# Kernel optimization log

Measured on AMD Instinct MI355X. Metric: run time of the kernel, lower is better.

## Reference

```python
import jax, jax.numpy as jnp
import numpy as np

B, T, V, DIN = 16, 360, 25, 2
H, NCLS, NAUX = 128, 12, 8
NSPLITS = NAUX + 1
N = T * V        # nodes per graph
E = 72000        # edges per graph
EPS = 1e-5       # BatchNorm eps


def _norm_coefs(edge_index, n):
    # GCNConv default: add self-loops, symmetric normalization D^-1/2 (A+I) D^-1/2
    src, dst = edge_index[0], edge_index[1]
    loops = jnp.arange(n, dtype=src.dtype)
    src = jnp.concatenate([src, loops])
    dst = jnp.concatenate([dst, loops])
    deg = jnp.zeros((n,), jnp.float32).at[dst].add(1.0)
    dinv = jax.lax.rsqrt(deg)
    return src, dst, dinv[src] * dinv[dst]


def _gcn_bn_relu(x, W, b, gamma, beta, src, dst, coef):
    # x: [B, N, din] -> [B, N, dout]; GCNConv then BatchNorm1d (batch stats) + ReLU
    h = x @ W
    msg = h[:, src, :] * coef[None, :, None]          # gather + scale
    agg = jnp.zeros(h.shape, h.dtype).at[:, dst, :].add(msg) + b  # scatter-add
    mean = agg.mean(axis=(0, 1))
    var = agg.var(axis=(0, 1))                        # biased var, as torch BN fwd
    hn = (agg - mean) * jax.lax.rsqrt(var + EPS)
    return jax.nn.relu(gamma * hn + beta)


def _head(x, Wg, bg, gamma, beta, Wf, bf, src, dst, coef):
    h = _gcn_bn_relu(x, Wg, bg, gamma, beta, src, dst, coef)
    pooled = h.mean(axis=1)                           # GlobalMeanPool (equal-size graphs)
    # Dropout is identity in eval mode
    return jax.nn.log_softmax(pooled @ Wf + bf, axis=1)


def setup_inputs() -> dict:
    key = jax.random.key(0)
    ks = jax.random.split(key, 8)
    s = 0.1
    return {
        "x": jax.random.normal(ks[0], (B, T, V, DIN), jnp.float32),
        "edge_index": jax.random.randint(ks[1], (2, E), 0, N, jnp.int64 if jax.config.jax_enable_x64 else jnp.int32),
        "W_in": jax.random.normal(ks[2], (DIN, H), jnp.float32) * s,
        "b_in": jnp.zeros((H,), jnp.float32),
        "g_in": jnp.ones((H,), jnp.float32),
        "be_in": jnp.zeros((H,), jnp.float32),
        "shared_W": jax.random.normal(ks[3], (2, H, H), jnp.float32) * s,
        "shared_b": jnp.zeros((2, H), jnp.float32),
        "shared_g": jnp.ones((2, H), jnp.float32),
        "shared_be": jnp.zeros((2, H), jnp.float32),
        "main_Wg": jax.random.normal(ks[4], (H, H), jnp.float32) * s,
        "main_bg": jnp.zeros((H,), jnp.float32),
        "main_g": jnp.ones((H,), jnp.float32),
        "main_be": jnp.zeros((H,), jnp.float32),
        "main_Wf": jax.random.normal(ks[5], (H, NCLS), jnp.float32) * s,
        "main_bf": jnp.zeros((NCLS,), jnp.float32),
        "aux_Wg": jax.random.normal(ks[6], (NAUX, H, H), jnp.float32) * s,
        "aux_bg": jnp.zeros((NAUX, H), jnp.float32),
        "aux_g": jnp.ones((NAUX, H), jnp.float32),
        "aux_be": jnp.zeros((NAUX, H), jnp.float32),
        "aux_Wf": jax.random.normal(ks[7], (NAUX, H, NCLS), jnp.float32) * s,
        "aux_bf": jnp.zeros((NAUX, NCLS), jnp.float32),
    }


def reference(x, edge_index, W_in, b_in, g_in, be_in, shared_W, shared_b, shared_g,
              shared_be, main_Wg, main_bg, main_g, main_be, main_Wf, main_bf,
              aux_Wg, aux_bg, aux_g, aux_be, aux_Wf, aux_bf):
    src, dst, coef = _norm_coefs(edge_index, N)
    h = x.reshape(B, N, DIN)
    h = _gcn_bn_relu(h, W_in, b_in, g_in, be_in, src, dst, coef)
    for i in range(shared_W.shape[0]):
        h = _gcn_bn_relu(h, shared_W[i], shared_b[i], shared_g[i], shared_be[i], src, dst, coef)
    o_main = _head(h, main_Wg, main_bg, main_g, main_be, main_Wf, main_bf, src, dst, coef)
    h4 = h.reshape(B, T, V, H)
    ws = T // NSPLITS
    t = jnp.arange(T)
    outs = []
    for i in range(NSPLITS - 1):
        idx = (t + ws * (i + 1)) % T          # cyclic time shift (fi[si:si+T])
        hr = h4[:, idx].reshape(B, N, H)
        outs.append(_head(hr, aux_Wg[i], aux_bg[i], aux_g[i], aux_be[i],
                          aux_Wf[i], aux_bf[i], src, dst, coef))
    o_aux = jnp.stack(outs, axis=1)           # [B, NAUX, NCLS]
    return o_main, o_aux
```

## Files before the change

### kernel.cpp

```cpp
#include <hip/hip_runtime.h>
#include <hip/hip_bf16.h>
#include <math.h>

#define BB 16
#define TT 360
#define VV 25
#define NN 9000
#define EE 72000
#define HH 128
#define RR (NN * BB)
#define CROWS 18000
#define NT128 1125
#define NPART0 563
#define NCLSS 12
#define EPSB 1e-5f


typedef _Float16 h8v __attribute__((ext_vector_type(8)));
typedef float float16v __attribute__((ext_vector_type(16)));

__device__ __forceinline__ h8v cf8(unsigned packed) {
    uint4 cc = {packed, packed, packed, packed};
    return __builtin_bit_cast(h8v, cc);
}


__global__ void k_count(const int* __restrict__ ei, int* __restrict__ counts) {
    int e = blockIdx.x * 256 + threadIdx.x;
    if (e < EE) atomicAdd(&counts[ei[EE + e]], 1);
}

__global__ void k_dinv(const int* __restrict__ counts, float* __restrict__ dinv,
                       unsigned* __restrict__ d2p) {
    int n = blockIdx.x * 256 + threadIdx.x;
    if (n >= NN) return;
    float di = rsqrtf((float)(counts[n] + 1));
    dinv[n] = di;
    _Float16 d2 = (_Float16)(di * di);
    unsigned short u = __builtin_bit_cast(unsigned short, d2);
    d2p[n] = (unsigned)u | ((unsigned)u << 16);
}

__global__ void k_scan(const int* __restrict__ counts, int* __restrict__ rowptr4) {
    __shared__ int part[1024];
    int t = threadIdx.x;
    int base = t * 9;
    int loc[9];
    int s = 0;
#pragma unroll
    for (int i = 0; i < 9; i++) {
        int idx = base + i;
        int v = (idx < NN) ? ((counts[idx] + 3) & ~3) : 0;
        loc[i] = s;
        s += v;
    }
    part[t] = s;
    __syncthreads();
    for (int d = 1; d < 1024; d <<= 1) {
        int v = (t >= d) ? part[t - d] : 0;
        __syncthreads();
        part[t] += v;
        __syncthreads();
    }
    int excl = (t == 0) ? 0 : part[t - 1];
#pragma unroll
    for (int i = 0; i < 9; i++) {
        int idx = base + i;
        if (idx < NN) rowptr4[idx] = excl + loc[i];
    }
    if (t == 1023) rowptr4[NN] = part[1023];
}

__global__ void k_fill(const int* __restrict__ ei, const int* __restrict__ rowptr4,
                       int* __restrict__ cursor, const float* __restrict__ dinv,
                       int2* __restrict__ csr) {
    int e = blockIdx.x * 256 + threadIdx.x;
    if (e >= EE) return;
    int s = ei[e], d = ei[EE + e];
    int slot = rowptr4[d] + atomicAdd(&cursor[d], 1);
    _Float16 cfh = (_Float16)(dinv[s] * dinv[d]);
    unsigned short u = __builtin_bit_cast(unsigned short, cfh);
    int2 e2;
    e2.x = s;
    e2.y = (int)((unsigned)u | ((unsigned)u << 16));
    csr[slot] = e2;
}

__global__ void k_pad(const int* __restrict__ rowptr4, const int* __restrict__ cursor,
                      int2* __restrict__ csr) {
    int n = blockIdx.x * 256 + threadIdx.x;
    if (n >= NN) return;
    int beg = rowptr4[n] + cursor[n];
    int end = rowptr4[n + 1];
    int2 z;
    z.x = n;
    z.y = 0;
    for (int e = beg; e < end; e++) csr[e] = z;
}

__global__ void k_wcvt(const float* __restrict__ sW, const float* __restrict__ mW,
                       const float* __restrict__ aW, _Float16* __restrict__ Wh) {
    int idx = blockIdx.x * 256 + threadIdx.x;
    if (idx >= 11 * 16384) return;
    int l = idx >> 14, r = idx & 16383;
    int k = r >> 7, c = r & 127;
    const float* src = (l < 2) ? sW + (size_t)l * 16384
                               : ((l == 2) ? mW : aW + (size_t)(l - 3) * 16384);
    Wh[(size_t)l * 16384 + c * 128 + k] = (_Float16)src[k * 128 + c];
}

__global__ void k_prop2(const float* __restrict__ x, float* __restrict__ P0,
                        const int* __restrict__ rowptr4, const int2* __restrict__ csr,
                        const float* __restrict__ dinv) {
    int n = blockIdx.x * 256 + threadIdx.x;
    if (n >= NN) return;
    int b = blockIdx.y;
    const float* xb = x + (size_t)b * NN * 2;
    float d2 = dinv[n] * dinv[n];
    float a0 = d2 * xb[2 * n], a1 = d2 * xb[2 * n + 1];
    int beg = rowptr4[n], end = rowptr4[n + 1];
    for (int j = beg; j < end; j++) {
        int2 e2 = csr[j];
        int s = e2.x;
        unsigned short u = (unsigned short)((unsigned)e2.y & 0xffffu);
        float cf = (float)__builtin_bit_cast(_Float16, u);
        a0 += cf * xb[2 * s];
        a1 += cf * xb[2 * s + 1];
    }
    float* Pb = P0 + (size_t)(n * BB + b) * 2;
    Pb[0] = a0;
    Pb[1] = a1;
}

__global__ void __launch_bounds__(256) k_mm2(const float* __restrict__ P0,
                                             _Float16* __restrict__ A,
                                             const float* __restrict__ W,
                                             const float* __restrict__ bias,
                                             float* __restrict__ pS1, float* __restrict__ pS2) {
    __shared__ float L1[256][8], L2[256][8];
    int t = threadIdx.x;
    int cg = t & 15, c8 = cg * 8;
    float wv0[8], wv1[8], bv[8];
#pragma unroll
    for (int j = 0; j < 8; j++) {
        wv0[j] = W[c8 + j];
        wv1[j] = W[HH + c8 + j];
        bv[j] = bias[c8 + j];
    }
    float s1[8], s2[8];
#pragma unroll
    for (int j = 0; j < 8; j++) { s1[j] = 0.f; s2[j] = 0.f; }
    for (int idx = blockIdx.x * 256 + t; idx < RR * 16; idx += gridDim.x * 256) {
        int Rr = idx >> 4;
        int q = Rr / CROWS;
        int rr = Rr - q * CROWS;
        int n = rr >> 1;
        int b = q * 2 + (rr & 1);
        float p0 = P0[((size_t)n * BB + b) * 2], p1 = P0[((size_t)n * BB + b) * 2 + 1];
        h8v o;
#pragma unroll
        for (int j = 0; j < 8; j++) {
            float v = p0 * wv0[j] + p1 * wv1[j] + bv[j];
            s1[j] += v;
            s2[j] += v * v;
            o[j] = (_Float16)v;
        }
        *(h8v*)(A + (size_t)Rr * HH + c8) = o;
    }
#pragma unroll
    for (int j = 0; j < 8; j++) { L1[t][j] = s1[j]; L2[t][j] = s2[j]; }
    __syncthreads();
    if (t < 16) {
#pragma unroll
        for (int g = 1; g < 16; g++)
#pragma unroll
            for (int j = 0; j < 8; j++) {
                s1[j] = (g == 1 ? L1[t][j] : s1[j]) + L1[t + 16 * g][j];
                s2[j] = (g == 1 ? L2[t][j] : s2[j]) + L2[t + 16 * g][j];
            }
#pragma unroll
        for (int j = 0; j < 8; j++) {
            pS1[(size_t)(t * 8 + j) * NPART0 + blockIdx.x] = s1[j];
            pS2[(size_t)(t * 8 + j) * NPART0 + blockIdx.x] = s2[j];
        }
    }
}

__global__ void __launch_bounds__(256) k_act(const _Float16* __restrict__ A,
                                             _Float16* __restrict__ HP,
                                             const float* __restrict__ scale,
                                             const float* __restrict__ shiftv) {
    int i = blockIdx.x * 256 + threadIdx.x;
    int c8 = (i & 15) * 8;
    h8v v = *(const h8v*)(A + (size_t)i * 8);
    h8v o;
#pragma unroll
    for (int j = 0; j < 8; j++) {
        float f = (float)v[j] * scale[c8 + j] + shiftv[c8 + j];
        o[j] = (_Float16)fmaxf(f, 0.f);
    }
    *(h8v*)(HP + (size_t)i * 8) = o;
}

__global__ void __launch_bounds__(256) k_gather1(const _Float16* __restrict__ h,
                                                 _Float16* __restrict__ Pz,
                                                 const int* __restrict__ rowptr4,
                                                 const int2* __restrict__ csr,
                                                 const unsigned* __restrict__ d2p) {
    int t = threadIdx.x;
    int q = blockIdx.x & 7;
    int ng4 = blockIdx.x >> 3;
    int wv = t >> 6, l = t & 63;
    int n = ng4 * 4 + wv;
    int half = l >> 5, li = l & 31;
    const _Float16* hb = h + (size_t)q * CROWS * HH + (size_t)li * 8;
    h8v acc;
    {
        h8v v = *(const h8v*)(hb + (size_t)n * 2 * HH);
        acc = v * cf8(half ? 0u : d2p[n]);
    }
    int beg = rowptr4[n], end = rowptr4[n + 1];
    int e = beg;
    for (; e + 8 <= end; e += 8) {
        int4 m0 = *(const int4*)(csr + e);
        int4 m1 = *(const int4*)(csr + e + 2);
        int4 m2 = *(const int4*)(csr + e + 4);
        int4 m3 = *(const int4*)(csr + e + 6);
        int s0 = half ? m0.z : m0.x;
        int s1 = half ? m1.z : m1.x;
        int s2 = half ? m2.z : m2.x;
        int s3 = half ? m3.z : m3.x;
        h8v v0 = *(const h8v*)(hb + (size_t)s0 * 2 * HH);
        h8v v1 = *(const h8v*)(hb + (size_t)s1 * 2 * HH);
        h8v v2 = *(const h8v*)(hb + (size_t)s2 * 2 * HH);
        h8v v3 = *(const h8v*)(hb + (size_t)s3 * 2 * HH);
        acc += v0 * cf8((unsigned)(half ? m0.w : m0.y));
        acc += v1 * cf8((unsigned)(half ? m1.w : m1.y));
        acc += v2 * cf8((unsigned)(half ? m2.w : m2.y));
        acc += v3 * cf8((unsigned)(half ? m3.w : m3.y));
    }
    if (e < end) {
        int4 m0 = *(const int4*)(csr + e);
        int4 m1 = *(const int4*)(csr + e + 2);
        int s0 = half ? m0.z : m0.x;
        int s1 = half ? m1.z : m1.x;
        h8v v0 = *(const h8v*)(hb + (size_t)s0 * 2 * HH);
        h8v v1 = *(const h8v*)(hb + (size_t)s1 * 2 * HH);
        acc += v0 * cf8((unsigned)(half ? m0.w : m0.y));
        acc += v1 * cf8((unsigned)(half ? m1.w : m1.y));
    }
    {
        int4 ai = __builtin_bit_cast(int4, acc);
        int4 bi4;
        bi4.x = __shfl_xor(ai.x, 32, 64);
        bi4.y = __shfl_xor(ai.y, 32, 64);
        bi4.z = __shfl_xor(ai.z, 32, 64);
        bi4.w = __shfl_xor(ai.w, 32, 64);
        acc += __builtin_bit_cast(h8v, bi4);
    }
    if (half == 0) {
        *(h8v*)(Pz + ((size_t)q * CROWS + (size_t)n * 2) * HH + (size_t)li * 8) = acc;
    }
}

__global__ void __launch_bounds__(256) k_gather3c(const _Float16* __restrict__ h,
                                                  _Float16* B0, _Float16* B1, _Float16* B2,
                                                  const int* __restrict__ rowptr4,
                                                  const int2* __restrict__ csr,
                                                  const unsigned* __restrict__ d2p,
                                                  int shbase) {
    int t = threadIdx.x;
    int q = blockIdx.x & 7;
    int ng4 = blockIdx.x >> 3;
    int wv = t >> 6, l = t & 63;
    int n = ng4 * 4 + wv;
    int half = l >> 5, li = l & 31;
    const _Float16* hb = h + (size_t)q * CROWS * HH + (size_t)li * 8;
    int sh0 = shbase, sh1 = shbase + 1000, sh2 = shbase + 2000;
    h8v acc0, acc1, acc2;
    {
        unsigned dp = half ? 0u : d2p[n];
        int p0 = n + sh0; if (p0 >= NN) p0 -= NN;
        int p1 = n + sh1; if (p1 >= NN) p1 -= NN;
        int p2 = n + sh2; if (p2 >= NN) p2 -= NN;
        h8v v0 = *(const h8v*)(hb + (size_t)p0 * 2 * HH);
        h8v v1 = *(const h8v*)(hb + (size_t)p1 * 2 * HH);
        h8v v2 = *(const h8v*)(hb + (size_t)p2 * 2 * HH);
        h8v dv = cf8(dp);
        acc0 = v0 * dv;
        acc1 = v1 * dv;
        acc2 = v2 * dv;
    }
    int beg = rowptr4[n], end = rowptr4[n + 1];
    for (int e = beg; e < end; e += 4) {
        int4 m0 = *(const int4*)(csr + e);
        int4 m1 = *(const int4*)(csr + e + 2);
        int sA = half ? m0.z : m0.x;
        int sB = half ? m1.z : m1.x;
        unsigned cA = (unsigned)(half ? m0.w : m0.y);
        unsigned cB = (unsigned)(half ? m1.w : m1.y);
        int a0 = sA + sh0; if (a0 >= NN) a0 -= NN;
        int a1 = sA + sh1; if (a1 >= NN) a1 -= NN;
        int a2 = sA + sh2; if (a2 >= NN) a2 -= NN;
        int b0 = sB + sh0; if (b0 >= NN) b0 -= NN;
        int b1 = sB + sh1; if (b1 >= NN) b1 -= NN;
        int b2 = sB + sh2; if (b2 >= NN) b2 -= NN;
        h8v vA0 = *(const h8v*)(hb + (size_t)a0 * 2 * HH);
        h8v vA1 = *(const h8v*)(hb + (size_t)a1 * 2 * HH);
        h8v vA2 = *(const h8v*)(hb + (size_t)a2 * 2 * HH);
        h8v vB0 = *(const h8v*)(hb + (size_t)b0 * 2 * HH);
        h8v vB1 = *(const h8v*)(hb + (size_t)b1 * 2 * HH);
        h8v vB2 = *(const h8v*)(hb + (size_t)b2 * 2 * HH);
        h8v fA = cf8(cA), fB = cf8(cB);
        acc0 += vA0 * fA;
        acc1 += vA1 * fA;
        acc2 += vA2 * fA;
        acc0 += vB0 * fB;
        acc1 += vB1 * fB;
        acc2 += vB2 * fB;
    }
#pragma unroll
    for (int z = 0; z < 3; z++) {
        h8v* ap = (z == 0) ? &acc0 : ((z == 1) ? &acc1 : &acc2);
        int4 ai = __builtin_bit_cast(int4, *ap);
        int4 bi4;
        bi4.x = __shfl_xor(ai.x, 32, 64);
        bi4.y = __shfl_xor(ai.y, 32, 64);
        bi4.z = __shfl_xor(ai.z, 32, 64);
        bi4.w = __shfl_xor(ai.w, 32, 64);
        *ap += __builtin_bit_cast(h8v, bi4);
    }
    if (half == 0) {
        size_t off = ((size_t)q * CROWS + (size_t)n * 2) * HH + (size_t)li * 8;
        *(h8v*)(B0 + off) = acc0;
        *(h8v*)(B1 + off) = acc1;
        *(h8v*)(B2 + off) = acc2;
    }
}

__global__ void __launch_bounds__(256) k_mfma3(_Float16* B0, _Float16* B1, _Float16* B2,
                                               const _Float16* __restrict__ Wh_g,
                                               const float* bias0, const float* bias1,
                                               const float* bias2,
                                               float* __restrict__ pS1,
                                               float* __restrict__ pS2) {
    __shared__ float rb1[4][128], rb2[4][128];
    int z = blockIdx.y;
    _Float16* B = (z == 0) ? B0 : ((z == 1) ? B1 : B2);
    const _Float16* Wh = Wh_g + (size_t)z * 16384;
    const float* bias = (z == 0) ? bias0 : ((z == 1) ? bias1 : bias2);
    int t = threadIdx.x;
    int w = t >> 6, l = t & 63;
    int rw = w >> 1, cw = w & 1;
    int lr = l & 31, hi = l >> 5;
    size_t rbase = (size_t)blockIdx.x * 128;
    const _Float16* Pr0 = B + (rbase + rw * 32 + lr) * HH + hi * 8;
    const _Float16* Pr1 = B + (rbase + 64 + rw * 32 + lr) * HH + hi * 8;
    const _Float16* Wc0 = Wh + (size_t)(cw * 64 + lr) * HH + hi * 8;
    const _Float16* Wc1 = Wh + (size_t)(cw * 64 + 32 + lr) * HH + hi * 8;
    float16v acc2[2][2];
#pragma unroll
    for (int rt = 0; rt < 2; rt++)
#pragma unroll
        for (int ct = 0; ct < 2; ct++) acc2[rt][ct] = (float16v)(0.0f);
    h8v a0 = *(const h8v*)(Pr0);
    h8v a1 = *(const h8v*)(Pr1);
    h8v b0 = *(const h8v*)(Wc0);
    h8v b1 = *(const h8v*)(Wc1);
#pragma unroll
    for (int ks = 0; ks < 8; ks++) {
        h8v a0n, a1n, b0n, b1n;
        if (ks < 7) {
            int koff = (ks + 1) * 16;
            a0n = *(const h8v*)(Pr0 + koff);
            a1n = *(const h8v*)(Pr1 + koff);
            b0n = *(const h8v*)(Wc0 + koff);
            b1n = *(const h8v*)(Wc1 + koff);
        }
        acc2[0][0] = __builtin_amdgcn_mfma_f32_32x32x16_f16(a0, b0, acc2[0][0], 0, 0, 0);
        acc2[0][1] = __builtin_amdgcn_mfma_f32_32x32x16_f16(a0, b1, acc2[0][1], 0, 0, 0);
        acc2[1][0] = __builtin_amdgcn_mfma_f32_32x32x16_f16(a1, b0, acc2[1][0], 0, 0, 0);
        acc2[1][1] = __builtin_amdgcn_mfma_f32_32x32x16_f16(a1, b1, acc2[1][1], 0, 0, 0);
        if (ks < 7) {
            a0 = a0n;
            a1 = a1n;
            b0 = b0n;
            b1 = b1n;
        }
    }
    __syncthreads();
    float bv[2] = {bias[cw * 64 + lr], bias[cw * 64 + 32 + lr]};
    float s1a[2] = {0.f, 0.f}, s2a[2] = {0.f, 0.f};
#pragma unroll
    for (int rt = 0; rt < 2; rt++)
#pragma unroll
        for (int ct = 0; ct < 2; ct++) {
            int c = cw * 64 + ct * 32 + lr;
#pragma unroll
            for (int g = 0; g < 16; g++) {
                int row = rt * 64 + rw * 32 + (g & 3) + 8 * (g >> 2) + 4 * hi;
                float v = acc2[rt][ct][g] + bv[ct];
                s1a[ct] += v;
                s2a[ct] += v * v;
                B[(rbase + row) * HH + c] = (_Float16)v;
            }
        }
    int slot = rw * 2 + hi;
#pragma unroll
    for (int ct = 0; ct < 2; ct++) {
        int cidx = cw * 64 + ct * 32 + lr;
        rb1[slot][cidx] = s1a[ct];
        rb2[slot][cidx] = s2a[ct];
    }
    __syncthreads();
    if (t < 128) {
        float a1r = rb1[0][t] + rb1[1][t] + rb1[2][t] + rb1[3][t];
        float a2r = rb2[0][t] + rb2[1][t] + rb2[2][t] + rb2[3][t];
        pS1[((size_t)z * HH + t) * NT128 + blockIdx.x] = a1r;
        pS2[((size_t)z * HH + t) * NT128 + blockIdx.x] = a2r;
    }
}

__global__ void __launch_bounds__(256) k_bnfin3(const float* __restrict__ pS1,
                                                const float* __restrict__ pS2, int npart,
                                                const float* g0, const float* g1,
                                                const float* g2, const float* be0,
                                                const float* be1, const float* be2,
                                                float* __restrict__ scale,
                                                float* __restrict__ shiftv) {
    __shared__ float R1[256], R2[256];
    int z = blockIdx.x >> 7, c = blockIdx.x & 127;
    const float* g = (z == 0) ? g0 : ((z == 1) ? g1 : g2);
    const float* be = (z == 0) ? be0 : ((z == 1) ? be1 : be2);
    int t = threadIdx.x;
    const float* p1 = pS1 + ((size_t)z * HH + c) * npart;
    const float* p2 = pS2 + ((size_t)z * HH + c) * npart;
    float s1 = 0.f, s2 = 0.f;
    for (int i = t; i < npart; i += 256) {
        s1 += p1[i];
        s2 += p2[i];
    }
    R1[t] = s1;
    R2[t] = s2;
    __syncthreads();
    for (int d = 128; d > 0; d >>= 1) {
        if (t < d) {
            R1[t] += R1[t + d];
            R2[t] += R2[t + d];
        }
        __syncthreads();
    }
    if (t == 0) {
        float inv = 1.0f / (float)RR;
        float mu = R1[0] * inv;
        float var = R2[0] * inv - mu * mu;
        float sc = g[c] * rsqrtf(var + EPSB);
        scale[z * HH + c] = sc;
        shiftv[z * HH + c] = be[c] - mu * sc;
    }
}

__global__ void __launch_bounds__(256) k_pool3(const _Float16* B0, const _Float16* B1,
                                               const _Float16* B2,
                                               const float* __restrict__ scale,
                                               const float* __restrict__ shiftv,
                                               float* __restrict__ pooled) {
    __shared__ float L[256][8];
    int z = blockIdx.y;
    const _Float16* A = (z == 0) ? B0 : ((z == 1) ? B1 : B2);
    const float* sc0 = scale + z * HH;
    const float* sh0 = shiftv + z * HH;
    float* pz = pooled + (size_t)z * BB * HH;
    int t = threadIdx.x;
    int q = blockIdx.x & 7;
    int rr = blockIdx.x >> 3;
    int par = rr & 1;
    int n0 = (rr >> 1) * 250;
    int b = q * 2 + par;
    int ng = t >> 4, c8 = (t & 15) * 8;
    float sc[8], sh[8];
#pragma unroll
    for (int j = 0; j < 8; j++) {
        sc[j] = sc0[c8 + j];
        sh[j] = sh0[c8 + j];
    }
    const _Float16* Ab = A + ((size_t)q * CROWS + par) * HH;
    float acc[8];
#pragma unroll
    for (int j = 0; j < 8; j++) acc[j] = 0.f;
    for (int n = n0 + ng; n < n0 + 250; n += 16) {
        h8v v = *(const h8v*)(Ab + (size_t)n * 2 * HH + c8);
#pragma unroll
        for (int j = 0; j < 8; j++) {
            float f = (float)v[j] * sc[j] + sh[j];
            acc[j] += fmaxf(f, 0.f);
        }
    }
#pragma unroll
    for (int j = 0; j < 8; j++) L[t][j] = acc[j];
    __syncthreads();
    if (ng == 0) {
#pragma unroll
        for (int g = 1; g < 16; g++)
#pragma unroll
            for (int j = 0; j < 8; j++) acc[j] += L[t + 16 * g][j];
#pragma unroll
        for (int j = 0; j < 8; j++) atomicAdd(&pz[b * HH + t * 8 + j], acc[j]);
    }
}

__global__ void __launch_bounds__(192) k_head_all(const float* __restrict__ pooled,
                                                  const float* __restrict__ main_Wf,
                                                  const float* __restrict__ main_bf,
                                                  const float* __restrict__ aux_Wf,
                                                  const float* __restrict__ aux_bf,
                                                  float* __restrict__ out) {
    int hd = blockIdx.x;
    const float* Wf = hd ? aux_Wf + (size_t)(hd - 1) * HH * NCLSS : main_Wf;
    const float* bf = hd ? aux_bf + (hd - 1) * NCLSS : main_bf;
    const float* pl = pooled + (size_t)hd * BB * HH;
    __shared__ float z[BB][NCLSS];
    __shared__ float lse[BB];
    int t = threadIdx.x;
    int b = t / NCLSS, j = t % NCLSS;
    if (t < BB * NCLSS) {
        float acc = bf[j];
        const float invn = 1.0f / NN;
        for (int c = 0; c < HH; c++) acc += pl[b * HH + c] * invn * Wf[c * NCLSS + j];
        z[b][j] = acc;
    }
    __syncthreads();
    if (t < BB) {
        float m = -1e30f;
        for (int j2 = 0; j2 < NCLSS; j2++) m = fmaxf(m, z[t][j2]);
        float s = 0.f;
        for (int j2 = 0; j2 < NCLSS; j2++) s += expf(z[t][j2] - m);
        lse[t] = m + logf(s);
    }
    __syncthreads();
    if (t < BB * NCLSS) {
        float* o = hd ? out + BB * NCLSS + ((size_t)b * 8 + (hd - 1)) * NCLSS + j
                      : out + b * NCLSS + j;
        *o = z[b][j] - lse[b];
    }
}


extern "C" void kernel_launch(void* const* d_in, const int* in_sizes, int n_in, void* d_out,
                              int out_size, void* d_ws, size_t ws_size, hipStream_t stream) {
    const float* x = (const float*)d_in[0];
    const int* ei = (const int*)d_in[1];
    const float* W_in = (const float*)d_in[2];
    const float* b_in = (const float*)d_in[3];
    const float* g_in = (const float*)d_in[4];
    const float* be_in = (const float*)d_in[5];
    const float* shared_W = (const float*)d_in[6];
    const float* shared_b = (const float*)d_in[7];
    const float* shared_g = (const float*)d_in[8];
    const float* shared_be = (const float*)d_in[9];
    const float* main_Wg = (const float*)d_in[10];
    const float* main_bg = (const float*)d_in[11];
    const float* main_g = (const float*)d_in[12];
    const float* main_be = (const float*)d_in[13];
    const float* main_Wf = (const float*)d_in[14];
    const float* main_bf = (const float*)d_in[15];
    const float* aux_Wg = (const float*)d_in[16];
    const float* aux_bg = (const float*)d_in[17];
    const float* aux_g = (const float*)d_in[18];
    const float* aux_be = (const float*)d_in[19];
    const float* aux_Wf = (const float*)d_in[20];
    const float* aux_bf = (const float*)d_in[21];
    float* out = (float*)d_out;

    char* w = (char*)d_ws;
    const size_t BIG = (size_t)RR * HH * 2;
    _Float16* U = (_Float16*)w;  w += BIG;
    _Float16* V = (_Float16*)w;  w += BIG;
    _Float16* P = (_Float16*)w;  w += BIG;
    _Float16* HP = (_Float16*)w; w += BIG;
    float* P0 = (float*)w;       w += (size_t)RR * 2 * 4;
    _Float16* Wh = (_Float16*)w; w += (size_t)11 * 16384 * 2;
    int2* csr = (int2*)w;        w += (size_t)102400 * 8;
    int* counts = (int*)w;       w += NN * 4;
    int* cursor = (int*)w;       w += NN * 4;
    float* dinv = (float*)w;     w += NN * 4;
    unsigned* d2p = (unsigned*)w; w += NN * 4;
    int* rowptr4 = (int*)w;      w += 36016;
    float* pS1 = (float*)w;      w += (size_t)3 * HH * NT128 * 4;
    float* pS2 = (float*)w;      w += (size_t)3 * HH * NT128 * 4;
    float* pooled = (float*)w;   w += 9 * BB * HH * 4;
    float* tscale = (float*)w;   w += 512;
    float* tshift = (float*)w;   w += 512;
    float* hscale = (float*)w;   w += 2048;
    float* hshift = (float*)w;   w += 2048;

    hipMemsetAsync(counts, 0, 2 * NN * 4, stream);
    hipMemsetAsync(pooled, 0, 9 * BB * HH * 4, stream);

    k_count<<<(EE + 255) / 256, 256, 0, stream>>>(ei, counts);
    k_dinv<<<(NN + 255) / 256, 256, 0, stream>>>(counts, dinv, d2p);
    k_scan<<<1, 1024, 0, stream>>>(counts, rowptr4);
    k_fill<<<(EE + 255) / 256, 256, 0, stream>>>(ei, rowptr4, cursor, dinv, csr);
    k_pad<<<(NN + 255) / 256, 256, 0, stream>>>(rowptr4, cursor, csr);
    k_wcvt<<<(11 * 16384 + 255) / 256, 256, 0, stream>>>(shared_W, main_Wg, aux_Wg, Wh);

    {
        dim3 g((NN + 255) / 256, BB);
        k_prop2<<<g, 256, 0, stream>>>(x, P0, rowptr4, csr, dinv);
        k_mm2<<<NPART0, 256, 0, stream>>>(P0, U, W_in, b_in, pS1, pS2);
        k_bnfin3<<<HH, 256, 0, stream>>>(pS1, pS2, NPART0, g_in, g_in, g_in, be_in, be_in,
                                         be_in, tscale, tshift);
    }

    k_act<<<RR * 16 / 256, 256, 0, stream>>>(U, HP, tscale, tshift);
    k_gather1<<<8 * 2250, 256, 0, stream>>>(HP, V, rowptr4, csr, d2p);
    k_mfma3<<<dim3(NT128, 1), 256, 0, stream>>>(V, V, V, Wh, shared_b, shared_b, shared_b,
                                                pS1, pS2);
    k_bnfin3<<<HH, 256, 0, stream>>>(pS1, pS2, NT128, shared_g, shared_g, shared_g, shared_be,
                                     shared_be, shared_be, tscale, tshift);
    k_act<<<RR * 16 / 256, 256, 0, stream>>>(V, HP, tscale, tshift);
    k_gather1<<<8 * 2250, 256, 0, stream>>>(HP, U, rowptr4, csr, d2p);
    k_mfma3<<<dim3(NT128, 1), 256, 0, stream>>>(U, U, U, Wh + 16384, shared_b + HH,
                                                shared_b + HH, shared_b + HH, pS1, pS2);
    k_bnfin3<<<HH, 256, 0, stream>>>(pS1, pS2, NT128, shared_g + HH, shared_g + HH,
                                     shared_g + HH, shared_be + HH, shared_be + HH,
                                     shared_be + HH, tscale, tshift);
    k_act<<<RR * 16 / 256, 256, 0, stream>>>(U, HP, tscale, tshift);

    for (int g = 0; g < 3; g++) {
        int h0 = g * 3;
        const float* bg[3];
        const float* gg[3];
        const float* be[3];
        for (int z = 0; z < 3; z++) {
            int hd = h0 + z;
            bg[z] = (hd == 0) ? main_bg : aux_bg + (hd - 1) * HH;
            gg[z] = (hd == 0) ? main_g : aux_g + (hd - 1) * HH;
            be[z] = (hd == 0) ? main_be : aux_be + (hd - 1) * HH;
        }
        k_gather3c<<<8 * 2250, 256, 0, stream>>>(HP, P, U, V, rowptr4, csr, d2p, h0 * 1000);
        k_mfma3<<<dim3(NT128, 3), 256, 0, stream>>>(P, U, V, Wh + (size_t)(2 + h0) * 16384,
                                                    bg[0], bg[1], bg[2], pS1, pS2);
        k_bnfin3<<<3 * HH, 256, 0, stream>>>(pS1, pS2, NT128, gg[0], gg[1], gg[2], be[0],
                                             be[1], be[2], hscale, hshift);
        k_pool3<<<dim3(576, 3), 256, 0, stream>>>(P, U, V, hscale, hshift,
                                                  pooled + (size_t)h0 * BB * HH);
    }
    k_head_all<<<9, 192, 0, stream>>>(pooled, main_Wf, main_bf, aux_Wf, aux_bf, out);
}
```

Before: 741.8 us.

## Split shifted 3-head gather into two column-half launches with four edge lanes

After: 792.3 us. +6.8%, slower.

```diff
diff --git a/kernel.cpp b/kernel.cpp
--- a/kernel.cpp
+++ b/kernel.cpp
@@ -22,6 +22,16 @@
 __device__ __forceinline__ h8v cf8(unsigned packed) {
     uint4 cc = {packed, packed, packed, packed};
     return __builtin_bit_cast(h8v, cc);
+}
+
+__device__ __forceinline__ h8v xadd(h8v a, int lanexor) {
+    int4 ai = __builtin_bit_cast(int4, a);
+    int4 bi;
+    bi.x = __shfl_xor(ai.x, lanexor, 64);
+    bi.y = __shfl_xor(ai.y, lanexor, 64);
+    bi.z = __shfl_xor(ai.z, lanexor, 64);
+    bi.w = __shfl_xor(ai.w, lanexor, 64);
+    return a + __builtin_bit_cast(h8v, bi);
 }
 
 
@@ -249,37 +259,31 @@
         acc += v0 * cf8((unsigned)(half ? m0.w : m0.y));
         acc += v1 * cf8((unsigned)(half ? m1.w : m1.y));
     }
-    {
-        int4 ai = __builtin_bit_cast(int4, acc);
-        int4 bi4;
-        bi4.x = __shfl_xor(ai.x, 32, 64);
-        bi4.y = __shfl_xor(ai.y, 32, 64);
-        bi4.z = __shfl_xor(ai.z, 32, 64);
-        bi4.w = __shfl_xor(ai.w, 32, 64);
-        acc += __builtin_bit_cast(h8v, bi4);
-    }
+    acc = xadd(acc, 32);
     if (half == 0) {
         *(h8v*)(Pz + ((size_t)q * CROWS + (size_t)n * 2) * HH + (size_t)li * 8) = acc;
     }
 }
 
-__global__ void __launch_bounds__(256) k_gather3c(const _Float16* __restrict__ h,
-                                                  _Float16* B0, _Float16* B1, _Float16* B2,
-                                                  const int* __restrict__ rowptr4,
-                                                  const int2* __restrict__ csr,
-                                                  const unsigned* __restrict__ d2p,
-                                                  int shbase) {
+__global__ void __launch_bounds__(256) k_gather3ch(const _Float16* __restrict__ h,
+                                                   _Float16* B0, _Float16* B1, _Float16* B2,
+                                                   const int* __restrict__ rowptr4,
+                                                   const int2* __restrict__ csr,
+                                                   const unsigned* __restrict__ d2p,
+                                                   int shbase, int H) {
     int t = threadIdx.x;
     int q = blockIdx.x & 7;
     int ng4 = blockIdx.x >> 3;
     int wv = t >> 6, l = t & 63;
     int n = ng4 * 4 + wv;
-    int half = l >> 5, li = l & 31;
-    const _Float16* hb = h + (size_t)q * CROWS * HH + (size_t)li * 8;
+    int q4 = l >> 4, li16 = l & 15;
+    int selhi = (l >> 5) & 1, sello = (l >> 4) & 1;
+    size_t loff = (size_t)(li16 >> 3) * HH + (size_t)H * 64 + (size_t)(li16 & 7) * 8;
+    const _Float16* hb = h + (size_t)q * CROWS * HH + loff;
     int sh0 = shbase, sh1 = shbase + 1000, sh2 = shbase + 2000;
     h8v acc0, acc1, acc2;
     {
-        unsigned dp = half ? 0u : d2p[n];
+        unsigned dp = (q4 == 0) ? d2p[n] : 0u;
         int p0 = n + sh0; if (p0 >= NN) p0 -= NN;
         int p1 = n + sh1; if (p1 >= NN) p1 -= NN;
         int p2 = n + sh2; if (p2 >= NN) p2 -= NN;
@@ -295,43 +299,25 @@
     for (int e = beg; e < end; e += 4) {
         int4 m0 = *(const int4*)(csr + e);
         int4 m1 = *(const int4*)(csr + e + 2);
-        int sA = half ? m0.z : m0.x;
-        int sB = half ? m1.z : m1.x;
-        unsigned cA = (unsigned)(half ? m0.w : m0.y);
-        unsigned cB = (unsigned)(half ? m1.w : m1.y);
-        int a0 = sA + sh0; if (a0 >= NN) a0 -= NN;
-        int a1 = sA + sh1; if (a1 >= NN) a1 -= NN;
-        int a2 = sA + sh2; if (a2 >= NN) a2 -= NN;
-        int b0 = sB + sh0; if (b0 >= NN) b0 -= NN;
-        int b1 = sB + sh1; if (b1 >= NN) b1 -= NN;
-        int b2 = sB + sh2; if (b2 >= NN) b2 -= NN;
-        h8v vA0 = *(const h8v*)(hb + (size_t)a0 * 2 * HH);
-        h8v vA1 = *(const h8v*)(hb + (size_t)a1 * 2 * HH);
-        h8v vA2 = *(const h8v*)(hb + (size_t)a2 * 2 * HH);
-        h8v vB0 = *(const h8v*)(hb + (size_t)b0 * 2 * HH);
-        h8v vB1 = *(const h8v*)(hb + (size_t)b1 * 2 * HH);
-        h8v vB2 = *(const h8v*)(hb + (size_t)b2 * 2 * HH);
-        h8v fA = cf8(cA), fB = cf8(cB);
-        acc0 += vA0 * fA;
-        acc1 += vA1 * fA;
-        acc2 += vA2 * fA;
-        acc0 += vB0 * fB;
-        acc1 += vB1 * fB;
-        acc2 += vB2 * fB;
-    }
-#pragma unroll
-    for (int z = 0; z < 3; z++) {
-        h8v* ap = (z == 0) ? &acc0 : ((z == 1) ? &acc1 : &acc2);
-        int4 ai = __builtin_bit_cast(int4, *ap);
-        int4 bi4;
-        bi4.x = __shfl_xor(ai.x, 32, 64);
-        bi4.y = __shfl_xor(ai.y, 32, 64);
-        bi4.z = __shfl_xor(ai.z, 32, 64);
-        bi4.w = __shfl_xor(ai.w, 32, 64);
-        *ap += __builtin_bit_cast(h8v, bi4);
-    }
-    if (half == 0) {
-        size_t off = ((size_t)q * CROWS + (size_t)n * 2) * HH + (size_t)li * 8;
+        int4 m = selhi ? m1 : m0;
+        int s = sello ? m.z : m.x;
+        unsigned cp = (unsigned)(sello ? m.w : m.y);
+        int a0 = s + sh0; if (a0 >= NN) a0 -= NN;
+        int a1 = s + sh1; if (a1 >= NN) a1 -= NN;
+        int a2 = s + sh2; if (a2 >= NN) a2 -= NN;
+        h8v v0 = *(const h8v*)(hb + (size_t)a0 * 2 * HH);
+        h8v v1 = *(const h8v*)(hb + (size_t)a1 * 2 * HH);
+        h8v v2 = *(const h8v*)(hb + (size_t)a2 * 2 * HH);
+        h8v f = cf8(cp);
+        acc0 += v0 * f;
+        acc1 += v1 * f;
+        acc2 += v2 * f;
+    }
+    acc0 = xadd(xadd(acc0, 16), 32);
+    acc1 = xadd(xadd(acc1, 16), 32);
+    acc2 = xadd(xadd(acc2, 16), 32);
+    if (q4 == 0) {
+        size_t off = ((size_t)q * CROWS + (size_t)n * 2) * HH + loff;
         *(h8v*)(B0 + off) = acc0;
         *(h8v*)(B1 + off) = acc1;
         *(h8v*)(B2 + off) = acc2;
@@ -638,7 +624,10 @@
             gg[z] = (hd == 0) ? main_g : aux_g + (hd - 1) * HH;
             be[z] = (hd == 0) ? main_be : aux_be + (hd - 1) * HH;
         }
-        k_gather3c<<<8 * 2250, 256, 0, stream>>>(HP, P, U, V, rowptr4, csr, d2p, h0 * 1000);
+        k_gather3ch<<<8 * 2250, 256, 0, stream>>>(HP, P, U, V, rowptr4, csr, d2p,
+                                                  h0 * 1000, 0);
+        k_gather3ch<<<8 * 2250, 256, 0, stream>>>(HP, P, U, V, rowptr4, csr, d2p,
+                                                  h0 * 1000, 1);
         k_mfma3<<<dim3(NT128, 3), 256, 0, stream>>>(P, U, V, Wh + (size_t)(2 + h0) * 16384,
                                                     bg[0], bg[1], bg[2], pS1, pS2);
         k_bnfin3<<<3 * HH, 256, 0, stream>>>(pS1, pS2, NT128, gg[0], gg[1], gg[2], be[0],
```
